# Kernel tuning notes

Hardware: AMD Instinct MI355X
Metric: run time of the kernel (lower is better)

Reference implementation:

```python
import jax, jax.numpy as jnp
import numpy as np

NUM_EMBEDDINGS = 1024
EMBEDDING_DIM = 32  # Z_NH
COMMITMENT_LOSS_FACTOR = 0.1
QUANTIZATION_LOSS_FACTOR = 0.1


def setup_inputs() -> dict:
    key = jax.random.key(0)
    k1, k2 = jax.random.split(key)
    h = jax.random.normal(k1, (256, 512, EMBEDDING_DIM), dtype=jnp.float32)
    # nn.Embedding weight init: uniform(-1/K, 1/K)
    embeddings = jax.random.uniform(
        k2, (NUM_EMBEDDINGS, EMBEDDING_DIM), dtype=jnp.float32,
        minval=-1.0 / NUM_EMBEDDINGS, maxval=1.0 / NUM_EMBEDDINGS)
    return {"h": h, "embeddings": embeddings}


def reference(h, embeddings):
    flat = h.reshape(-1, EMBEDDING_DIM)                       # [N, D]
    dist = ((flat ** 2).sum(-1, keepdims=True)
            + (embeddings ** 2).sum(-1)
            - 2.0 * flat @ embeddings.T)                      # [N, K]
    idx = jnp.argmin(dist, axis=-1)                           # [N]
    # one_hot @ weight == direct row gather
    quantized = embeddings[idx].reshape(h.shape)              # [B, S, D]
    q_flat = quantized.reshape(-1, EMBEDDING_DIM)
    commitment_loss = jnp.mean((jax.lax.stop_gradient(q_flat) - flat) ** 2, axis=-1)
    embedding_loss = jnp.mean((q_flat - jax.lax.stop_gradient(flat)) ** 2, axis=-1)
    # straight-through estimator
    quantized_st = h + jax.lax.stop_gradient(quantized - h)
    loss = (commitment_loss * COMMITMENT_LOSS_FACTOR
            + embedding_loss * QUANTIZATION_LOSS_FACTOR)      # [N]
    quantized_indices = idx[:, None]                          # [N, 1]
    return quantized_st, quantized_indices, loss
```

## Files before the change

### kernel.cpp

```cpp
#include <hip/hip_runtime.h>


#define EMB_N 1024
#define DIM 32
#define NVEC (256 * 512)
#define NTILES (EMB_N / 16)
#define NT_LDS 36
#define MAXC 8

typedef unsigned long long u64;
typedef unsigned int u32;
typedef unsigned short ushortT;
typedef __attribute__((ext_vector_type(8))) short bf16x8;
typedef __attribute__((ext_vector_type(4))) float f32x4;

__device__ __forceinline__ u32 enc_f32(float x) {
    u32 u = __float_as_uint(x);
    return (u & 0x80000000u) ? ~u : (u | 0x80000000u);
}
__device__ __forceinline__ ushortT f2bf(float f) {
    u32 u = __float_as_uint(f);
    return (ushortT)((u + 0x7FFFu + ((u >> 16) & 1u)) >> 16);
}
__device__ __forceinline__ u64 shflx_u64(u64 x, int m) {
    int lo = __shfl_xor((int)(u32)x, m);
    int hi = __shfl_xor((int)(x >> 32), m);
    return ((u64)(u32)hi << 32) | (u32)lo;
}

__device__ __forceinline__ float norm2_np(const float* fr) {
    float sq[DIM];
#pragma unroll
    for (int i = 0; i < DIM; ++i) sq[i] = fr[i] * fr[i];
    float r[8];
#pragma unroll
    for (int j = 0; j < 8; ++j)
        r[j] = ((sq[j] + sq[j + 8]) + sq[j + 16]) + sq[j + 24];
    return ((r[0] + r[1]) + (r[2] + r[3])) + ((r[4] + r[5]) + (r[6] + r[7]));
}

__global__ __launch_bounds__(256) void prep_kernel(
    const float* __restrict__ emb, float* __restrict__ e2,
    ushortT* __restrict__ bfrag)
{
#pragma clang fp contract(off)
    const int t = blockIdx.x * 256 + threadIdx.x;
    const int l = t & 63;
    const int row = ((t >> 6) << 4) + (l & 15);
    const int k0 = (l >> 4) * 8;
    const float* ep = emb + (size_t)row * DIM + k0;
    ushortT* dst = bfrag + (size_t)t * 8;
#pragma unroll
    for (int j = 0; j < 8; ++j) dst[j] = f2bf(ep[j]);
    if (t < EMB_N) {
        const float* e = emb + (size_t)t * DIM;
        float tmp[DIM];
#pragma unroll
        for (int i = 0; i < DIM; ++i) tmp[i] = e[i];
        e2[t] = norm2_np(tmp);
    }
}

#define S1BODY(BEXPR, NT) do {                                                  \
    bf16x8 b = *(const bf16x8*)(BEXPR);                                         \
    f32x4 d0 = __builtin_amdgcn_mfma_f32_16x16x32_bf16(afr0, b, zacc, 0, 0, 0); \
    f32x4 d1 = __builtin_amdgcn_mfma_f32_16x16x32_bf16(afr1, b, zacc, 0, 0, 0); \
    float e2c = e2[(NT) * 16 + col16];                                          \
    _Pragma("unroll")                                                           \
    for (int r = 0; r < 4; ++r) {                                               \
        bs[r]     = fminf(bs[r],     __builtin_fmaf(-2.f, d0[r], e2c));         \
        bs[4 + r] = fminf(bs[4 + r], __builtin_fmaf(-2.f, d1[r], e2c));         \
    }                                                                           \
} while (0)

#define S2BODY(BEXPR, NT) do {                                                  \
    bf16x8 b = *(const bf16x8*)(BEXPR);                                         \
    f32x4 d0 = __builtin_amdgcn_mfma_f32_16x16x32_bf16(afr0, b, zacc, 0, 0, 0); \
    f32x4 d1 = __builtin_amdgcn_mfma_f32_16x16x32_bf16(afr1, b, zacc, 0, 0, 0); \
    float e2c = e2[(NT) * 16 + col16];                                          \
    const u32 cc = (NT) * 16 + col16;                                           \
    bool q[8];                                                                  \
    bool any = false;                                                           \
    _Pragma("unroll")                                                           \
    for (int i = 0; i < 8; ++i) {                                               \
        float s = __builtin_fmaf(-2.f, ((i >> 2) ? d1[i & 3] : d0[i & 3]), e2c);\
        q[i] = (s <= thr[i]);                                                   \
        any |= q[i];                                                            \
    }                                                                           \
    if (__ballot(any)) {                                                        \
        _Pragma("unroll")                                                       \
        for (int i = 0; i < 8; ++i) {                                           \
            if (__ballot(q[i])) {                                               \
                if (q[i]) {                                                     \
                    const int rloc = ((i >> 2) << 4) + quad * 4 + (i & 3);      \
                    u32 slot = atomicAdd(&cnt[rloc], 1u);                       \
                    if (slot < MAXC) cand[rloc * MAXC + slot] = (ushortT)cc;    \
                }                                                               \
            }                                                                   \
        }                                                                       \
    }                                                                           \
} while (0)

__global__ __launch_bounds__(256) void vq_scan(
    const float* __restrict__ h,
    const float* __restrict__ emb,
    const float* __restrict__ e2,
    const ushortT* __restrict__ bfrag,
    float* __restrict__ out_q, float* __restrict__ out_idx,
    float* __restrict__ out_loss)
{
#pragma clang fp contract(off)
    __shared__ __align__(16) ushortT s_b[NT_LDS * 512];
    __shared__ u32     lds_cnt[4][32];
    __shared__ ushortT lds_cand[4][32 * MAXC];

    {
        const uint4* src = (const uint4*)bfrag;
        uint4* dst = (uint4*)s_b;
        for (int o = threadIdx.x; o < NT_LDS * 64; o += 256) dst[o] = src[o];
    }

    const int wslot = threadIdx.x >> 6;
    const int wid   = (blockIdx.x * 256 + threadIdx.x) >> 6;
    const int lane  = threadIdx.x & 63;
    const int col16 = lane & 15;
    const int quad  = lane >> 4;
    const size_t row0 = (size_t)wid * 32;

    u32*     cnt  = lds_cnt[wslot];
    ushortT* cand = lds_cand[wslot];
    if (lane < 32) cnt[lane] = 0;

    bf16x8 afr0, afr1;
    float sa0, sa1;
    {
        const float* ap = h + (row0 + col16) * DIM + quad * 8;
        float4 x = *(const float4*)ap, y = *(const float4*)(ap + 4);
        afr0[0]=(short)f2bf(x.x); afr0[1]=(short)f2bf(x.y); afr0[2]=(short)f2bf(x.z); afr0[3]=(short)f2bf(x.w);
        afr0[4]=(short)f2bf(y.x); afr0[5]=(short)f2bf(y.y); afr0[6]=(short)f2bf(y.z); afr0[7]=(short)f2bf(y.w);
        sa0 = fabsf(x.x)+fabsf(x.y)+fabsf(x.z)+fabsf(x.w)+fabsf(y.x)+fabsf(y.y)+fabsf(y.z)+fabsf(y.w);
        const float* bp = ap + 16 * DIM;
        float4 u = *(const float4*)bp, v = *(const float4*)(bp + 4);
        afr1[0]=(short)f2bf(u.x); afr1[1]=(short)f2bf(u.y); afr1[2]=(short)f2bf(u.z); afr1[3]=(short)f2bf(u.w);
        afr1[4]=(short)f2bf(v.x); afr1[5]=(short)f2bf(v.y); afr1[6]=(short)f2bf(v.z); afr1[7]=(short)f2bf(v.w);
        sa1 = fabsf(u.x)+fabsf(u.y)+fabsf(u.z)+fabsf(u.w)+fabsf(v.x)+fabsf(v.y)+fabsf(v.z)+fabsf(v.w);
    }
    sa0 += __shfl_xor(sa0, 16); sa0 += __shfl_xor(sa0, 32);
    sa1 += __shfl_xor(sa1, 16); sa1 += __shfl_xor(sa1, 32);

    __syncthreads();

    const f32x4 zacc = {0.f, 0.f, 0.f, 0.f};

    float bs[8];
#pragma unroll
    for (int i = 0; i < 8; ++i) bs[i] = 3.4e38f;
#pragma unroll 2
    for (int nt = 0; nt < NT_LDS; ++nt)
        S1BODY(s_b + nt * 512 + lane * 8, nt);
#pragma unroll 2
    for (int nt = NT_LDS; nt < NTILES; ++nt)
        S1BODY(bfrag + nt * 512 + lane * 8, nt);
#pragma unroll
    for (int m = 1; m < 16; m <<= 1)
#pragma unroll
        for (int i = 0; i < 8; ++i) bs[i] = fminf(bs[i], __shfl_xor(bs[i], m));

    float thr[8];
#pragma unroll
    for (int i = 0; i < 8; ++i) {
        float sar = __shfl((i >> 2) ? sa1 : sa0, quad * 4 + (i & 3));
        thr[i] = bs[i] + __builtin_fmaf(sar, 0x1p-16f, 1.0e-4f);
    }

#pragma unroll 2
    for (int nt = 0; nt < NT_LDS; ++nt)
        S2BODY(s_b + nt * 512 + lane * 8, nt);
#pragma unroll 2
    for (int nt = NT_LDS; nt < NTILES; ++nt)
        S2BODY(bfrag + nt * 512 + lane * 8, nt);

    u64 ovf = __ballot((lane < 32) && (cnt[lane & 31] > MAXC));
    while (ovf) {
        const int r = (int)(__ffsll((unsigned long long)ovf) - 1);
        ovf &= ovf - 1;
        const float* fp = h + (row0 + r) * DIM;
        float fu[DIM];
#pragma unroll
        for (int i = 0; i < DIM; i += 4) {
            float4 x = *(const float4*)(fp + i);
            fu[i] = x.x; fu[i + 1] = x.y; fu[i + 2] = x.z; fu[i + 3] = x.w;
        }
        const float f2 = norm2_np(fu);
        u64 bk = ~0ull;
        for (int c = lane; c < EMB_N; c += 64) {
            const float* ep = emb + (size_t)c * DIM;
            float a = 0.f;
#pragma unroll
            for (int k = 0; k < DIM; ++k) a = __builtin_fmaf(fu[k], ep[k], a);
            float dd = (f2 + e2[c]) - (2.0f * a);
            u64 key = ((u64)enc_f32(dd) << 32) | (u32)c;
            if (key < bk) bk = key;
        }
#pragma unroll
        for (int m = 1; m < 64; m <<= 1) {
            u64 o = shflx_u64(bk, m);
            if (o < bk) bk = o;
        }
        if (lane == 0) { cand[r * MAXC] = (ushortT)(bk & 1023u); cnt[r] = 1; }
    }

    if (lane < 32) {
        const int row = (int)row0 + lane;
        const u32 n = cnt[lane];
        const float* f = h + (size_t)row * DIM;
        float fr[DIM];
#pragma unroll
        for (int i = 0; i < DIM; i += 4) {
            float4 x = *(const float4*)(f + i);
            fr[i] = x.x; fr[i + 1] = x.y; fr[i + 2] = x.z; fr[i + 3] = x.w;
        }
        int bidx;
        if (n == 1) {
            bidx = (int)cand[lane * MAXC];
        } else {
            const float f2 = norm2_np(fr);
            u64 best = ~0ull;
            for (u32 j = 0; j < n; ++j) {
                const u32 c = (u32)cand[lane * MAXC + j];
                const float* ep = emb + (size_t)c * DIM;
                float a = 0.f;
#pragma unroll
                for (int k = 0; k < DIM; ++k) a = __builtin_fmaf(fr[k], ep[k], a);
                float dd = (f2 + e2[c]) - (2.0f * a);
                u64 key = ((u64)enc_f32(dd) << 32) | c;
                if (key < best) best = key;
            }
            bidx = (int)(best & 0xFFFFFFFFu);
        }

        const float* qv = emb + (size_t)bidx * DIM;
        float ps = 0.f;
#pragma unroll
        for (int i = 0; i < DIM; i += 4) {
            float4 qx; qx.x = qv[i]; qx.y = qv[i+1]; qx.z = qv[i+2]; qx.w = qv[i+3];
            float dx = qx.x - fr[i], dy = qx.y - fr[i+1], dz = qx.z - fr[i+2], dw = qx.w - fr[i+3];
            ps += dx * dx; ps += dy * dy; ps += dz * dz; ps += dw * dw;
            float4 o;
            o.x = fr[i]     + (qx.x - fr[i]);
            o.y = fr[i + 1] + (qx.y - fr[i + 1]);
            o.z = fr[i + 2] + (qx.z - fr[i + 2]);
            o.w = fr[i + 3] + (qx.w - fr[i + 3]);
            *(float4*)(out_q + (size_t)row * DIM + i) = o;
        }
        float m = ps * (1.0f / DIM);
        out_idx[row]  = (float)bidx;
        out_loss[row] = m * 0.1f + m * 0.1f;
    }
}

__global__ void e2_kernel(const float* __restrict__ emb, float* __restrict__ e2) {
#pragma clang fp contract(off)
    int c = blockIdx.x * blockDim.x + threadIdx.x;
    if (c >= EMB_N) return;
    const float* e = emb + (size_t)c * DIM;
    float tmp[DIM];
#pragma unroll
    for (int i = 0; i < DIM; ++i) tmp[i] = e[i];
    e2[c] = norm2_np(tmp);
}

__global__ __launch_bounds__(256) void vq_kernel(
    const float* __restrict__ h, const float* __restrict__ emb,
    const float* __restrict__ e2, float* __restrict__ out_q,
    float* __restrict__ out_idx, float* __restrict__ out_loss)
{
#pragma clang fp contract(off)
    const int v = blockIdx.x * blockDim.x + threadIdx.x;
    const float* f = h + (size_t)v * DIM;
    float fr[DIM];
#pragma unroll
    for (int i = 0; i < DIM; i += 4) {
        float4 x = *(const float4*)(f + i);
        fr[i] = x.x; fr[i + 1] = x.y; fr[i + 2] = x.z; fr[i + 3] = x.w;
    }
    const float f2 = norm2_np(fr);
    float best = 3.4e38f; int bidx = 0;
#pragma unroll 1
    for (int c = 0; c < EMB_N; ++c) {
        const float* e = emb + (size_t)c * DIM;
        float a0 = 0.f;
#pragma unroll
        for (int k = 0; k < DIM; ++k) a0 = __builtin_fmaf(fr[k], e[k], a0);
        float d0 = (f2 + e2[c]) - (2.0f * a0);
        if (d0 < best) { best = d0; bidx = c; }
    }
    const float* q = emb + (size_t)bidx * DIM;
    float ps = 0.f;
#pragma unroll
    for (int i = 0; i < DIM; i += 4) {
        float4 qx; qx.x = q[i]; qx.y = q[i+1]; qx.z = q[i+2]; qx.w = q[i+3];
        float dx = qx.x - fr[i], dy = qx.y - fr[i+1], dz = qx.z - fr[i+2], dw = qx.w - fr[i+3];
        ps += dx * dx; ps += dy * dy; ps += dz * dz; ps += dw * dw;
        float4 o;
        o.x = fr[i] + (qx.x - fr[i]); o.y = fr[i+1] + (qx.y - fr[i+1]);
        o.z = fr[i+2] + (qx.z - fr[i+2]); o.w = fr[i+3] + (qx.w - fr[i+3]);
        *(float4*)(out_q + (size_t)v * DIM + i) = o;
    }
    float m = ps * (1.0f / DIM);
    out_idx[v]  = (float)bidx;
    out_loss[v] = m * 0.1f + m * 0.1f;
}

extern "C" void kernel_launch(void* const* d_in, const int* in_sizes, int n_in,
                              void* d_out, int out_size, void* d_ws, size_t ws_size,
                              hipStream_t stream) {
    const float* h   = (const float*)d_in[0];
    const float* emb = (const float*)d_in[1];
    float* out = (float*)d_out;
    float* out_q    = out;
    float* out_idx  = out + (size_t)NVEC * DIM;
    float* out_loss = out + (size_t)NVEC * DIM + NVEC;

    float*   e2    = (float*)d_ws;
    ushortT* bfrag = (ushortT*)((char*)d_ws + 4096);
    const size_t need = 4096 + (size_t)EMB_N * DIM * sizeof(ushortT);

    if (ws_size >= need) {
        prep_kernel<<<16, 256, 0, stream>>>(emb, e2, bfrag);
        vq_scan<<<1024, 256, 0, stream>>>(h, emb, e2, bfrag,
                                          out_q, out_idx, out_loss);
    } else {
        e2_kernel<<<EMB_N / 256, 256, 0, stream>>>(emb, e2);
        vq_kernel<<<NVEC / 256, 256, 0, stream>>>(h, emb, e2, out_q, out_idx, out_loss);
    }
}
```

Before: 126.0 us.

## Bound min threshold from a codebook subset and prefetch B fragments in filter pass

The first pass now computes the per-row approximate minimum over only the first 16 codebook tiles instead of all 64, giving a looser upper-bound threshold for the candidate-filter pass. That removes most of the first MFMA sweep. In exchange, more candidates pass the filter, so the candidate capacity is raised from 8 to 10 to keep the exact-fallback overflow path rare. The second pass is also software-pipelined, loading the next two B fragments (from LDS or global) before processing the current pair to hide load latency.

```diff
diff --git a/kernel.cpp b/kernel.cpp
--- a/kernel.cpp
+++ b/kernel.cpp
@@ -6,7 +6,8 @@
 #define NVEC (256 * 512)
 #define NTILES (EMB_N / 16)
 #define NT_LDS 36
-#define MAXC 8
+#define NT_PRE 16
+#define MAXC 10
 
 typedef unsigned long long u64;
 typedef unsigned int u32;
@@ -61,10 +62,12 @@
     }
 }
 
-#define S1BODY(BEXPR, NT) do {                                                  \
-    bf16x8 b = *(const bf16x8*)(BEXPR);                                         \
-    f32x4 d0 = __builtin_amdgcn_mfma_f32_16x16x32_bf16(afr0, b, zacc, 0, 0, 0); \
-    f32x4 d1 = __builtin_amdgcn_mfma_f32_16x16x32_bf16(afr1, b, zacc, 0, 0, 0); \
+#define LDSB(J) (*(const bf16x8*)(s_b + (J) * 512 + lane * 8))
+#define GLBB(J) (*(const bf16x8*)(bfrag + (size_t)(J) * 512 + lane * 8))
+
+#define S1PROC(BVAL, NT) do {                                                   \
+    f32x4 d0 = __builtin_amdgcn_mfma_f32_16x16x32_bf16(afr0, (BVAL), zacc, 0, 0, 0); \
+    f32x4 d1 = __builtin_amdgcn_mfma_f32_16x16x32_bf16(afr1, (BVAL), zacc, 0, 0, 0); \
     float e2c = e2[(NT) * 16 + col16];                                          \
     _Pragma("unroll")                                                           \
     for (int r = 0; r < 4; ++r) {                                               \
@@ -73,10 +76,9 @@
     }                                                                           \
 } while (0)
 
-#define S2BODY(BEXPR, NT) do {                                                  \
-    bf16x8 b = *(const bf16x8*)(BEXPR);                                         \
-    f32x4 d0 = __builtin_amdgcn_mfma_f32_16x16x32_bf16(afr0, b, zacc, 0, 0, 0); \
-    f32x4 d1 = __builtin_amdgcn_mfma_f32_16x16x32_bf16(afr1, b, zacc, 0, 0, 0); \
+#define S2PROC(BVAL, NT) do {                                                   \
+    f32x4 d0 = __builtin_amdgcn_mfma_f32_16x16x32_bf16(afr0, (BVAL), zacc, 0, 0, 0); \
+    f32x4 d1 = __builtin_amdgcn_mfma_f32_16x16x32_bf16(afr1, (BVAL), zacc, 0, 0, 0); \
     float e2c = e2[(NT) * 16 + col16];                                          \
     const u32 cc = (NT) * 16 + col16;                                           \
     bool q[8];                                                                  \
@@ -156,11 +158,10 @@
 #pragma unroll
     for (int i = 0; i < 8; ++i) bs[i] = 3.4e38f;
 #pragma unroll 2
-    for (int nt = 0; nt < NT_LDS; ++nt)
-        S1BODY(s_b + nt * 512 + lane * 8, nt);
-#pragma unroll 2
-    for (int nt = NT_LDS; nt < NTILES; ++nt)
-        S1BODY(bfrag + nt * 512 + lane * 8, nt);
+    for (int nt = 0; nt < NT_PRE; ++nt) {
+        bf16x8 b = LDSB(nt);
+        S1PROC(b, nt);
+    }
 #pragma unroll
     for (int m = 1; m < 16; m <<= 1)
 #pragma unroll
@@ -173,12 +174,26 @@
         thr[i] = bs[i] + __builtin_fmaf(sar, 0x1p-16f, 1.0e-4f);
     }
 
-#pragma unroll 2
-    for (int nt = 0; nt < NT_LDS; ++nt)
-        S2BODY(s_b + nt * 512 + lane * 8, nt);
-#pragma unroll 2
-    for (int nt = NT_LDS; nt < NTILES; ++nt)
-        S2BODY(bfrag + nt * 512 + lane * 8, nt);
+    {
+        bf16x8 pA = LDSB(0), pB = LDSB(1);
+        for (int nt = 0; nt < NT_LDS; nt += 2) {
+            const int f0 = nt + 2, f1 = nt + 3;
+            bf16x8 nA, nB;
+            if (f0 < NT_LDS) { nA = LDSB(f0); nB = LDSB(f1); }
+            else             { nA = GLBB(f0); nB = GLBB(f1); }
+            S2PROC(pA, nt);
+            S2PROC(pB, nt + 1);
+            pA = nA; pB = nB;
+        }
+        for (int nt = NT_LDS; nt < NTILES; nt += 2) {
+            const int f0 = (nt + 2 < NTILES) ? nt + 2 : nt;
+            const int f1 = (nt + 3 < NTILES) ? nt + 3 : nt + 1;
+            bf16x8 nA = GLBB(f0), nB = GLBB(f1);
+            S2PROC(pA, nt);
+            S2PROC(pB, nt + 1);
+            pA = nA; pB = nB;
+        }
+    }
 
     u64 ovf = __ballot((lane < 32) && (cnt[lane & 31] > MAXC));
     while (ovf) {
```

Result: slower. 382.9 us (+203.9%).
